# Kernel optimization log

Hardware: AMD Instinct MI355X
Metric: run time of the kernel (lower is better)

## Reference

```python
import jax, jax.numpy as jnp
import numpy as np

GRID = 2          # grid_num
IN_CH = 8         # mask branch out channels
CH = 8            # mask head channels
MR = 2.0          # mapping_ratio
SOI = jnp.array([64.0, 128.0, 256.0, 512.0, 1024.0], dtype=jnp.float32)


def _interp_matrix(out_len, in_len, dtype):
    # bilinear, align_corners=True, separable 1-D interpolation matrix [out_len, in_len]
    pos = jnp.arange(out_len, dtype=dtype) * ((in_len - 1) / (out_len - 1))
    lo = jnp.clip(jnp.floor(pos).astype(jnp.int32), 0, in_len - 2)
    frac = pos - lo.astype(dtype)
    M = jnp.zeros((out_len, in_len), dtype)
    idx = jnp.arange(out_len)
    M = M.at[idx, lo].add(1.0 - frac)
    M = M.at[idx, lo + 1].add(frac)
    return M


def _forward(mask_feats, mask_head_params, instance_locations, im_inds, fpn_levels, mask_feat_stride):
    N, C, H, W = mask_feats.shape
    n_inst = mask_head_params.shape[0]
    dt = mask_feats.dtype

    # compute_locations (FCOS): pixel centers of stride-s grid, (x, y) order, y-major flatten
    s = mask_feat_stride
    shifts_x = jnp.arange(W, dtype=dt) * s + s // 2
    shifts_y = jnp.arange(H, dtype=dt) * s + s // 2
    yy, xx = jnp.meshgrid(shifts_y, shifts_x, indexing='ij')
    locations = jnp.stack([xx.reshape(-1), yy.reshape(-1)], axis=-1)  # [H*W, 2]

    # relative coords, normalized by size-of-interest of each instance's FPN level
    rel = instance_locations[:, None, :] - locations[None, :, :]          # [n, HW, 2]
    rel = jnp.transpose(rel, (0, 2, 1))                                   # [n, 2, HW]
    rel = (rel / SOI[fpn_levels][:, None, None]).astype(dt)

    feats = mask_feats[im_inds].reshape(n_inst, IN_CH, H * W)             # [n, 8, HW]
    x = jnp.concatenate([rel, feats], axis=1).reshape(n_inst, IN_CH + 2, H, W)

    # grid-cell index from instance center (stride-8 coords, floor division)
    nl = instance_locations / 8.0
    gx = jnp.floor(jnp.clip(nl[:, 0], 0, W - 1) / (W // GRID))
    gy = jnp.floor(jnp.clip(nl[:, 1], 0, H - 1) / (H // GRID))
    loc_ind = (gx + GRID * gy).astype(jnp.int32)                          # [n]

    ih, iw = H // GRID, W // GRID
    # [n, c, gy, ih, gx, iw] -> [n, gy*gx, c, ih, iw], then gather one cell per instance
    xg = x.reshape(n_inst, IN_CH + 2, GRID, ih, GRID, iw)
    xg = jnp.transpose(xg, (0, 2, 4, 1, 3, 5)).reshape(n_inst, GRID * GRID, IN_CH + 2, ih, iw)
    x = xg[jnp.arange(n_inst), loc_ind]                                   # [n, 10, ih, iw]

    # parse dynamic params: weights [80, 64, 8] then biases [8, 8, 1]
    p = mask_head_params
    w0 = p[:, 0:80].reshape(n_inst, CH, IN_CH + 2)
    w1 = p[:, 80:144].reshape(n_inst, CH, CH)
    w2 = p[:, 144:152].reshape(n_inst, 1, CH)
    b0 = p[:, 152:160]
    b1 = p[:, 160:168]
    b2 = p[:, 168:169]

    # per-instance 1x1 grouped convs (groups = n_inst) as batched matmuls
    x = jax.nn.relu(jnp.einsum('nchw,nkc->nkhw', x, w0) + b0[:, :, None, None])
    x = jax.nn.relu(jnp.einsum('nchw,nkc->nkhw', x, w1) + b1[:, :, None, None])
    x = jnp.einsum('nchw,nkc->nkhw', x, w2) + b2[:, :, None, None]        # [n, 1, ih, iw]

    # bilinear upsample (align_corners=True) to out_size = (MR/2*H, MR/2*W) = (H, W)
    out_h = int(MR / 2.0 * H + 0.5)
    out_w = int(MR / 2.0 * W + 0.5)
    Mh = _interp_matrix(out_h, ih, dt)
    Mw = _interp_matrix(out_w, iw, dt)
    x = jnp.einsum('nchw,Hh,Ww->ncHW', x, Mh, Mw)
    return jax.nn.sigmoid(x)


def setup_inputs() -> dict:
    key = jax.random.key(0)
    k1, k2, k3, k4, k5 = jax.random.split(key, 5)
    N, H, W = 2, 192, 256
    n_inst = 128
    mask_feats = jax.random.normal(k1, (N, IN_CH, H, W), jnp.float32)
    mask_head_params = jax.random.normal(k2, (n_inst, 169), jnp.float32) * 0.1
    instance_locations = jax.random.uniform(k3, (n_inst, 2), jnp.float32) * jnp.array([W * 8.0, H * 8.0], jnp.float32)
    im_inds = jax.random.randint(k4, (n_inst,), 0, N)
    fpn_levels = jax.random.randint(k5, (n_inst,), 0, 5)
    return {
        'mask_feats': mask_feats,
        'mask_head_params': mask_head_params,
        'instance_locations': instance_locations,
        'im_inds': im_inds,
        'fpn_levels': fpn_levels,
        'mask_feat_stride': 8,
    }


def reference(mask_feats, mask_head_params, instance_locations, im_inds, fpn_levels, mask_feat_stride):
    return _forward(mask_feats, mask_head_params, instance_locations, im_inds, fpn_levels, mask_feat_stride)
```

## Files before the change

### kernel.cpp

```cpp
#include <hip/hip_runtime.h>


#define HH 192
#define WW 256
#define IH 96
#define IW 128
#define HW (HH * WW)

__global__ __launch_bounds__(256, 6) void dmh_kernel(
    const float* __restrict__ mf,
    const float* __restrict__ params,
    const float* __restrict__ locs,
    const int*   __restrict__ im_inds,
    const int*   __restrict__ fpn,
    const int*   __restrict__ stride_p,
    float*       __restrict__ out)
{
    __shared__ float m[8 * IW];

    const int bx   = blockIdx.x;
    const int inst = bx >> 4;
    const int q    = bx & 15;
    const int tid  = threadIdx.x;

    const int   s   = stride_p[0];
    const int   sh  = s >> 1;
    const float ix  = locs[2 * inst + 0];
    const float iy  = locs[2 * inst + 1];
    const float inv_soi = 1.0f / (float)(64 << fpn[inst]);
    const int   im  = im_inds[inst];

    const float nlx = ix * 0.125f;
    const float nly = iy * 0.125f;
    const int gx = (int)floorf(fminf(fmaxf(nlx, 0.0f), (float)(WW - 1)) / (float)(WW / 2));
    const int gy = (int)floorf(fminf(fmaxf(nly, 0.0f), (float)(HH - 1)) / (float)(HH / 2));

    const float* __restrict__ p = params + inst * 169;

    const int orow0 = q * 12;
    const int ms    = (int)((float)orow0 * (95.0f / 191.0f));

    {
        const int col4 = (tid & 31) * 4;
        const int r    = tid >> 5;
        int gr = ms + r; if (gr > IH - 1) gr = IH - 1;
        const int h = gy * IH + gr;
        const float rely = (iy - (float)(h * s + sh)) * inv_soi;

        const float* fbase = mf + (size_t)(im * 8) * HW + (size_t)h * WW
                             + gx * IW + col4;
        float4 f[8];
        #pragma unroll
        for (int c = 0; c < 8; ++c)
            f[c] = *(const float4*)(fbase + (size_t)c * HW);

        float4 res;
        float* rv = &res.x;
        #pragma unroll
        for (int j = 0; j < 4; ++j) {
            const float relx = (ix - (float)((gx * IW + col4 + j) * s + sh)) * inv_soi;
            float a[8];
            #pragma unroll
            for (int k = 0; k < 8; ++k) {
                float acc = p[152 + k];
                acc = fmaf(p[k * 10 + 0], relx, acc);
                acc = fmaf(p[k * 10 + 1], rely, acc);
                #pragma unroll
                for (int c = 0; c < 8; ++c)
                    acc = fmaf(p[k * 10 + 2 + c], ((const float*)&f[c])[j], acc);
                a[k] = fmaxf(acc, 0.0f);
            }
            float b[8];
            #pragma unroll
            for (int k = 0; k < 8; ++k) {
                float acc = p[160 + k];
                #pragma unroll
                for (int c = 0; c < 8; ++c)
                    acc = fmaf(p[80 + k * 8 + c], a[c], acc);
                b[k] = fmaxf(acc, 0.0f);
            }
            float acc = p[168];
            #pragma unroll
            for (int c = 0; c < 8; ++c)
                acc = fmaf(p[144 + c], b[c], acc);
            rv[j] = acc;
        }
        *(float4*)&m[r * IW + col4] = res;
    }
    __syncthreads();

    {
        const int ocol = tid;
        const float wpos = (float)ocol * (127.0f / 255.0f);
        int wlo = (int)wpos; if (wlo > IW - 2) wlo = IW - 2;
        const float fw = wpos - (float)wlo;

        float* op = out + (size_t)inst * HW + (size_t)orow0 * WW + ocol;

        #pragma unroll
        for (int r = 0; r < 12; ++r) {
            const float hpos = (float)(orow0 + r) * (95.0f / 191.0f);
            int hlo = (int)hpos; if (hlo > IH - 2) hlo = IH - 2;
            const float fh = hpos - (float)hlo;
            const int rl = hlo - ms;

            const float* mp = &m[rl * IW + wlo];
            const float v00 = mp[0];
            const float v01 = mp[1];
            const float v10 = mp[IW];
            const float v11 = mp[IW + 1];

            const float top = fmaf(fw, v01 - v00, v00);
            const float bot = fmaf(fw, v11 - v10, v10);
            const float val = fmaf(fh, bot - top, top);

            op[(size_t)r * WW] = 1.0f / (1.0f + __expf(-val));
        }
    }
}

extern "C" void kernel_launch(void* const* d_in, const int* in_sizes, int n_in,
                              void* d_out, int out_size, void* d_ws, size_t ws_size,
                              hipStream_t stream) {
    const float* mf       = (const float*)d_in[0];
    const float* params   = (const float*)d_in[1];
    const float* locs     = (const float*)d_in[2];
    const int*   im_inds  = (const int*)d_in[3];
    const int*   fpn      = (const int*)d_in[4];
    const int*   stride_p = (const int*)d_in[5];
    float*       out      = (float*)d_out;

    dmh_kernel<<<dim3(2048), dim3(256), 0, stream>>>(
        mf, params, locs, im_inds, fpn, stride_p, out);
}
```

Before: 20.57 us.

## Split dynamic mask head into separate MLP and upsample kernels via workspace

Replaces the fused kernel with two kernels when workspace allows: one computes the per-instance low-resolution mask with the MLP and writes it to the workspace, the other bilinearly upsamples it and applies sigmoid, using float4 stores. This removes the redundant MLP recomputation of overlapping low-res rows across the 16 row-chunks of the fused version. The cost is an extra launch and a round-trip of a 6 MB intermediate through global memory. The fallback fused kernel now processes two pixels per thread over eight rows.

```diff
diff --git a/kernel.cpp b/kernel.cpp
--- a/kernel.cpp
+++ b/kernel.cpp
@@ -6,114 +6,187 @@
 #define IH 96
 #define IW 128
 #define HW (HH * WW)
-
-__global__ __launch_bounds__(256, 6) void dmh_kernel(
-    const float* __restrict__ mf,
-    const float* __restrict__ params,
-    const float* __restrict__ locs,
-    const int*   __restrict__ im_inds,
-    const int*   __restrict__ fpn,
-    const int*   __restrict__ stride_p,
-    float*       __restrict__ out)
-{
-    __shared__ float m[8 * IW];
-
-    const int bx   = blockIdx.x;
-    const int inst = bx >> 4;
-    const int q    = bx & 15;
-    const int tid  = threadIdx.x;
-
-    const int   s   = stride_p[0];
-    const int   sh  = s >> 1;
-    const float ix  = locs[2 * inst + 0];
-    const float iy  = locs[2 * inst + 1];
-    const float inv_soi = 1.0f / (float)(64 << fpn[inst]);
-    const int   im  = im_inds[inst];
-
+#define MHW (IH * IW)
+
+__device__ __forceinline__ void inst_setup(
+    const float* __restrict__ locs, const int* __restrict__ im_inds,
+    const int* __restrict__ fpn, int s, int inst,
+    float& ix, float& iy, float& inv_soi, int& im, int& gx, int& gy)
+{
+    ix = locs[2 * inst + 0];
+    iy = locs[2 * inst + 1];
+    inv_soi = 1.0f / (float)(64 << fpn[inst]);
+    im = im_inds[inst];
     const float nlx = ix * 0.125f;
     const float nly = iy * 0.125f;
-    const int gx = (int)floorf(fminf(fmaxf(nlx, 0.0f), (float)(WW - 1)) / (float)(WW / 2));
-    const int gy = (int)floorf(fminf(fmaxf(nly, 0.0f), (float)(HH - 1)) / (float)(HH / 2));
-
+    gx = (int)floorf(fminf(fmaxf(nlx, 0.0f), (float)(WW - 1)) / (float)(WW / 2));
+    gy = (int)floorf(fminf(fmaxf(nly, 0.0f), (float)(HH - 1)) / (float)(HH / 2));
+}
+
+__device__ __forceinline__ float mlp_px(
+    const float* __restrict__ p, const float* f, float relx, float rely)
+{
+    float a[8];
+    #pragma unroll
+    for (int k = 0; k < 8; ++k) {
+        float acc = p[152 + k];
+        acc = fmaf(p[k * 10 + 0], relx, acc);
+        acc = fmaf(p[k * 10 + 1], rely, acc);
+        #pragma unroll
+        for (int c = 0; c < 8; ++c)
+            acc = fmaf(p[k * 10 + 2 + c], f[c], acc);
+        a[k] = fmaxf(acc, 0.0f);
+    }
+    float b[8];
+    #pragma unroll
+    for (int k = 0; k < 8; ++k) {
+        float acc = p[160 + k];
+        #pragma unroll
+        for (int c = 0; c < 8; ++c)
+            acc = fmaf(p[80 + k * 8 + c], a[c], acc);
+        b[k] = fmaxf(acc, 0.0f);
+    }
+    float acc = p[168];
+    #pragma unroll
+    for (int c = 0; c < 8; ++c)
+        acc = fmaf(p[144 + c], b[c], acc);
+    return acc;
+}
+
+__global__ __launch_bounds__(256, 8) void dmh_mask(
+    const float* __restrict__ mf, const float* __restrict__ params,
+    const float* __restrict__ locs, const int* __restrict__ im_inds,
+    const int* __restrict__ fpn, const int* __restrict__ stride_p,
+    float* __restrict__ mask)
+{
+    const int inst = blockIdx.y;
+    const int tid  = threadIdx.x;
+    const int s    = stride_p[0];
+    const int sh   = s >> 1;
+
+    float ix, iy, inv_soi; int im, gx, gy;
+    inst_setup(locs, im_inds, fpn, s, inst, ix, iy, inv_soi, im, gx, gy);
     const float* __restrict__ p = params + inst * 169;
 
+    const int col2 = (tid & 63) * 2;
+    const int gr   = blockIdx.x * 4 + (tid >> 6);
+    const int h    = gy * IH + gr;
+    const float rely = (iy - (float)(h * s + sh)) * inv_soi;
+
+    const float* fbase = mf + ((size_t)(im * 8) * HH + h) * WW + gx * IW + col2;
+    float2 f2[8];
+    #pragma unroll
+    for (int c = 0; c < 8; ++c)
+        f2[c] = *(const float2*)(fbase + (size_t)c * HW);
+
+    float f0[8], f1[8];
+    #pragma unroll
+    for (int c = 0; c < 8; ++c) { f0[c] = f2[c].x; f1[c] = f2[c].y; }
+
+    const float relx0 = (ix - (float)((gx * IW + col2) * s + sh)) * inv_soi;
+    const float relx1 = relx0 - (float)s * inv_soi;
+
+    float2 res;
+    res.x = mlp_px(p, f0, relx0, rely);
+    res.y = mlp_px(p, f1, relx1, rely);
+
+    *(float2*)&mask[(size_t)inst * MHW + gr * IW + col2] = res;
+}
+
+__global__ __launch_bounds__(256, 8) void dmh_upsample(
+    const float* __restrict__ mask, float* __restrict__ out)
+{
+    const int inst = blockIdx.y;
+    const int tid  = threadIdx.x;
+    const int col4 = (tid & 63) * 4;
+    const int orow = blockIdx.x * 4 + (tid >> 6);
+
+    const float hpos = (float)orow * (95.0f / 191.0f);
+    int hlo = (int)hpos; if (hlo > IH - 2) hlo = IH - 2;
+    const float fh = hpos - (float)hlo;
+
+    const float* mrow = mask + (size_t)inst * MHW + hlo * IW;
+
+    float4 v;
+    float* vv = &v.x;
+    #pragma unroll
+    for (int j = 0; j < 4; ++j) {
+        const float wpos = (float)(col4 + j) * (127.0f / 255.0f);
+        int wlo = (int)wpos; if (wlo > IW - 2) wlo = IW - 2;
+        const float fw = wpos - (float)wlo;
+
+        const float v00 = mrow[wlo];
+        const float v01 = mrow[wlo + 1];
+        const float v10 = mrow[wlo + IW];
+        const float v11 = mrow[wlo + IW + 1];
+
+        const float top = fmaf(fw, v01 - v00, v00);
+        const float bot = fmaf(fw, v11 - v10, v10);
+        const float val = fmaf(fh, bot - top, top);
+        vv[j] = 1.0f / (1.0f + __expf(-val));
+    }
+    *(float4*)(out + (size_t)inst * HW + (size_t)orow * WW + col4) = v;
+}
+
+__global__ __launch_bounds__(256, 6) void dmh_fused(
+    const float* __restrict__ mf, const float* __restrict__ params,
+    const float* __restrict__ locs, const int* __restrict__ im_inds,
+    const int* __restrict__ fpn, const int* __restrict__ stride_p,
+    float* __restrict__ out)
+{
+    __shared__ float m[8 * IW];
+    const int bx = blockIdx.x;
+    const int inst = bx >> 4;
+    const int q = bx & 15;
+    const int tid = threadIdx.x;
+    const int s = stride_p[0];
+    const int sh = s >> 1;
+
+    float ix, iy, inv_soi; int im, gx, gy;
+    inst_setup(locs, im_inds, fpn, s, inst, ix, iy, inv_soi, im, gx, gy);
+    const float* __restrict__ p = params + inst * 169;
+
     const int orow0 = q * 12;
-    const int ms    = (int)((float)orow0 * (95.0f / 191.0f));
-
+    const int ms = (int)((float)orow0 * (95.0f / 191.0f));
     {
-        const int col4 = (tid & 31) * 4;
-        const int r    = tid >> 5;
-        int gr = ms + r; if (gr > IH - 1) gr = IH - 1;
-        const int h = gy * IH + gr;
-        const float rely = (iy - (float)(h * s + sh)) * inv_soi;
-
-        const float* fbase = mf + (size_t)(im * 8) * HW + (size_t)h * WW
-                             + gx * IW + col4;
-        float4 f[8];
-        #pragma unroll
-        for (int c = 0; c < 8; ++c)
-            f[c] = *(const float4*)(fbase + (size_t)c * HW);
-
-        float4 res;
-        float* rv = &res.x;
-        #pragma unroll
-        for (int j = 0; j < 4; ++j) {
-            const float relx = (ix - (float)((gx * IW + col4 + j) * s + sh)) * inv_soi;
-            float a[8];
+        const int col2 = (tid & 63) * 2;
+        const int r = tid >> 6;
+        #pragma unroll
+        for (int rr = 0; rr < 2; ++rr) {
+            int gr = ms + r + rr * 4; if (gr > IH - 1) gr = IH - 1;
+            const int h = gy * IH + gr;
+            const float rely = (iy - (float)(h * s + sh)) * inv_soi;
+            const float* fbase = mf + ((size_t)(im * 8) * HH + h) * WW + gx * IW + col2;
+            float f0[8], f1[8];
             #pragma unroll
-            for (int k = 0; k < 8; ++k) {
-                float acc = p[152 + k];
-                acc = fmaf(p[k * 10 + 0], relx, acc);
-                acc = fmaf(p[k * 10 + 1], rely, acc);
-                #pragma unroll
-                for (int c = 0; c < 8; ++c)
-                    acc = fmaf(p[k * 10 + 2 + c], ((const float*)&f[c])[j], acc);
-                a[k] = fmaxf(acc, 0.0f);
+            for (int c = 0; c < 8; ++c) {
+                float2 t = *(const float2*)(fbase + (size_t)c * HW);
+                f0[c] = t.x; f1[c] = t.y;
             }
-            float b[8];
-            #pragma unroll
-            for (int k = 0; k < 8; ++k) {
-                float acc = p[160 + k];
-                #pragma unroll
-                for (int c = 0; c < 8; ++c)
-                    acc = fmaf(p[80 + k * 8 + c], a[c], acc);
-                b[k] = fmaxf(acc, 0.0f);
-            }
-            float acc = p[168];
-            #pragma unroll
-            for (int c = 0; c < 8; ++c)
-                acc = fmaf(p[144 + c], b[c], acc);
-            rv[j] = acc;
+            const float relx0 = (ix - (float)((gx * IW + col2) * s + sh)) * inv_soi;
+            const float relx1 = relx0 - (float)s * inv_soi;
+            m[(r + rr * 4) * IW + col2]     = mlp_px(p, f0, relx0, rely);
+            m[(r + rr * 4) * IW + col2 + 1] = mlp_px(p, f1, relx1, rely);
         }
-        *(float4*)&m[r * IW + col4] = res;
     }
     __syncthreads();
-
     {
         const int ocol = tid;
         const float wpos = (float)ocol * (127.0f / 255.0f);
         int wlo = (int)wpos; if (wlo > IW - 2) wlo = IW - 2;
         const float fw = wpos - (float)wlo;
-
         float* op = out + (size_t)inst * HW + (size_t)orow0 * WW + ocol;
-
         #pragma unroll
         for (int r = 0; r < 12; ++r) {
             const float hpos = (float)(orow0 + r) * (95.0f / 191.0f);
             int hlo = (int)hpos; if (hlo > IH - 2) hlo = IH - 2;
             const float fh = hpos - (float)hlo;
             const int rl = hlo - ms;
-
             const float* mp = &m[rl * IW + wlo];
-            const float v00 = mp[0];
-            const float v01 = mp[1];
-            const float v10 = mp[IW];
-            const float v11 = mp[IW + 1];
-
+            const float v00 = mp[0], v01 = mp[1], v10 = mp[IW], v11 = mp[IW + 1];
             const float top = fmaf(fw, v01 - v00, v00);
             const float bot = fmaf(fw, v11 - v10, v10);
             const float val = fmaf(fh, bot - top, top);
-
             op[(size_t)r * WW] = 1.0f / (1.0f + __expf(-val));
         }
     }
@@ -130,6 +203,14 @@
     const int*   stride_p = (const int*)d_in[5];
     float*       out      = (float*)d_out;
 
-    dmh_kernel<<<dim3(2048), dim3(256), 0, stream>>>(
-        mf, params, locs, im_inds, fpn, stride_p, out);
-}
+    const size_t mask_bytes = (size_t)128 * MHW * sizeof(float);
+    if (ws_size >= mask_bytes) {
+        float* mask = (float*)d_ws;
+        dmh_mask<<<dim3(24, 128), dim3(256), 0, stream>>>(
+            mf, params, locs, im_inds, fpn, stride_p, mask);
+        dmh_upsample<<<dim3(48, 128), dim3(256), 0, stream>>>(mask, out);
+    } else {
+        dmh_fused<<<dim3(2048), dim3(256), 0, stream>>>(
+            mf, params, locs, im_inds, fpn, stride_p, out);
+    }
+}
```

Result: slower. 28.66 us (+39.3%).

## Process 24 output rows per block to cut halo recompute of the MLP

Applied to the files above, without the earlier changes.

Each block now covers 24 output rows (14 source rows) instead of 12 output rows (8 source rows), halving the grid. The per-pixel MLP is no longer recomputed for the overlapping halo rows that adjacent blocks shared. The upsampling loop keeps the two interpolation rows in registers and reloads from shared memory only when the source row advances. In exchange there is less parallelism (1024 blocks), a partial second compute pass in which some threads sit idle, and a lower occupancy hint in launch bounds.

```diff
diff --git a/kernel.cpp b/kernel.cpp
--- a/kernel.cpp
+++ b/kernel.cpp
@@ -7,7 +7,7 @@
 #define IW 128
 #define HW (HH * WW)
 
-__global__ __launch_bounds__(256, 6) void dmh_kernel(
+__global__ __launch_bounds__(256, 4) void dmh_kernel(
     const float* __restrict__ mf,
     const float* __restrict__ params,
     const float* __restrict__ locs,
@@ -16,11 +16,11 @@
     const int*   __restrict__ stride_p,
     float*       __restrict__ out)
 {
-    __shared__ float m[8 * IW];
+    __shared__ float m[14 * IW];
 
     const int bx   = blockIdx.x;
-    const int inst = bx >> 4;
-    const int q    = bx & 15;
+    const int inst = bx >> 3;
+    const int j    = bx & 7;
     const int tid  = threadIdx.x;
 
     const int   s   = stride_p[0];
@@ -37,55 +37,67 @@
 
     const float* __restrict__ p = params + inst * 169;
 
-    const int orow0 = q * 12;
-    const int ms    = (int)((float)orow0 * (95.0f / 191.0f));
+    const int orow0 = j * 24;
+    const int ms    = (orow0 * 95) / 191;
 
     {
         const int col4 = (tid & 31) * 4;
-        const int r    = tid >> 5;
-        int gr = ms + r; if (gr > IH - 1) gr = IH - 1;
-        const int h = gy * IH + gr;
-        const float rely = (iy - (float)(h * s + sh)) * inv_soi;
+        const int rs   = tid >> 5;
+        const float relx0 = (ix - (float)((gx * IW + col4) * s + sh)) * inv_soi;
+        const float dstep = (float)s * inv_soi;
+        const float* fcol = mf + (size_t)(im * 8) * HW + gx * IW + col4;
 
-        const float* fbase = mf + (size_t)(im * 8) * HW + (size_t)h * WW
-                             + gx * IW + col4;
-        float4 f[8];
         #pragma unroll
-        for (int c = 0; c < 8; ++c)
-            f[c] = *(const float4*)(fbase + (size_t)c * HW);
+        for (int pass = 0; pass < 2; ++pass) {
+            const int r = rs + pass * 8;
+            if (r < 14) {
+                int gr = ms + r; if (gr > IH - 1) gr = IH - 1;
+                const int h = gy * IH + gr;
+                const float rely = (iy - (float)(h * s + sh)) * inv_soi;
 
-        float4 res;
-        float* rv = &res.x;
-        #pragma unroll
-        for (int j = 0; j < 4; ++j) {
-            const float relx = (ix - (float)((gx * IW + col4 + j) * s + sh)) * inv_soi;
-            float a[8];
-            #pragma unroll
-            for (int k = 0; k < 8; ++k) {
-                float acc = p[152 + k];
-                acc = fmaf(p[k * 10 + 0], relx, acc);
-                acc = fmaf(p[k * 10 + 1], rely, acc);
+                const float* fbase = fcol + (size_t)h * WW;
+                float4 F[8];
                 #pragma unroll
                 for (int c = 0; c < 8; ++c)
-                    acc = fmaf(p[k * 10 + 2 + c], ((const float*)&f[c])[j], acc);
-                a[k] = fmaxf(acc, 0.0f);
+                    F[c] = *(const float4*)(fbase + (size_t)c * HW);
+
+                float4 res;
+                float* rv = &res.x;
+                #pragma unroll
+                for (int jp = 0; jp < 4; ++jp) {
+                    const float relx = relx0 - (float)jp * dstep;
+                    float f[8];
+                    #pragma unroll
+                    for (int c = 0; c < 8; ++c) f[c] = ((const float*)&F[c])[jp];
+                    float a[8];
+                    #pragma unroll
+                    for (int k = 0; k < 8; ++k) {
+                        float acc = p[152 + k];
+                        acc = fmaf(p[k * 10 + 0], relx, acc);
+                        acc = fmaf(p[k * 10 + 1], rely, acc);
+                        #pragma unroll
+                        for (int c = 0; c < 8; ++c)
+                            acc = fmaf(p[k * 10 + 2 + c], f[c], acc);
+                        a[k] = fmaxf(acc, 0.0f);
+                    }
+                    float b[8];
+                    #pragma unroll
+                    for (int k = 0; k < 8; ++k) {
+                        float acc = p[160 + k];
+                        #pragma unroll
+                        for (int c = 0; c < 8; ++c)
+                            acc = fmaf(p[80 + k * 8 + c], a[c], acc);
+                        b[k] = fmaxf(acc, 0.0f);
+                    }
+                    float acc = p[168];
+                    #pragma unroll
+                    for (int c = 0; c < 8; ++c)
+                        acc = fmaf(p[144 + c], b[c], acc);
+                    rv[jp] = acc;
+                }
+                *(float4*)&m[r * IW + col4] = res;
             }
-            float b[8];
-            #pragma unroll
-            for (int k = 0; k < 8; ++k) {
-                float acc = p[160 + k];
-                #pragma unroll
-                for (int c = 0; c < 8; ++c)
-                    acc = fmaf(p[80 + k * 8 + c], a[c], acc);
-                b[k] = fmaxf(acc, 0.0f);
-            }
-            float acc = p[168];
-            #pragma unroll
-            for (int c = 0; c < 8; ++c)
-                acc = fmaf(p[144 + c], b[c], acc);
-            rv[j] = acc;
         }
-        *(float4*)&m[r * IW + col4] = res;
     }
     __syncthreads();
 
@@ -97,23 +109,36 @@
 
         float* op = out + (size_t)inst * HW + (size_t)orow0 * WW + ocol;
 
-        #pragma unroll
-        for (int r = 0; r < 12; ++r) {
-            const float hpos = (float)(orow0 + r) * (95.0f / 191.0f);
-            int hlo = (int)hpos; if (hlo > IH - 2) hlo = IH - 2;
-            const float fh = hpos - (float)hlo;
-            const int rl = hlo - ms;
-
-            const float* mp = &m[rl * IW + wlo];
-            const float v00 = mp[0];
-            const float v01 = mp[1];
-            const float v10 = mp[IW];
-            const float v11 = mp[IW + 1];
-
+        float v00 = m[wlo];
+        float v01 = m[wlo + 1];
+        float v10 = m[IW + wlo];
+        float v11 = m[IW + wlo + 1];
+        int cur = 0;
+        {
+            const float fh = (float)orow0 * (95.0f / 191.0f) - (float)ms;
             const float top = fmaf(fw, v01 - v00, v00);
             const float bot = fmaf(fw, v11 - v10, v10);
             const float val = fmaf(fh, bot - top, top);
+            op[0] = 1.0f / (1.0f + __expf(-val));
+        }
 
+        #pragma unroll
+        for (int r = 1; r < 24; ++r) {
+            const int orow = orow0 + r;
+            int ihlo = (orow * 95) / 191;
+            if (ihlo > IH - 2) ihlo = IH - 2;
+            const float fh = (float)orow * (95.0f / 191.0f) - (float)ihlo;
+            const int rl = ihlo - ms;
+
+            if (rl != cur) {
+                v00 = v10; v01 = v11;
+                v10 = m[(rl + 1) * IW + wlo];
+                v11 = m[(rl + 1) * IW + wlo + 1];
+                cur = rl;
+            }
+            const float top = fmaf(fw, v01 - v00, v00);
+            const float bot = fmaf(fw, v11 - v10, v10);
+            const float val = fmaf(fh, bot - top, top);
             op[(size_t)r * WW] = 1.0f / (1.0f + __expf(-val));
         }
     }
@@ -130,6 +155,6 @@
     const int*   stride_p = (const int*)d_in[5];
     float*       out      = (float*)d_out;
 
-    dmh_kernel<<<dim3(2048), dim3(256), 0, stream>>>(
+    dmh_kernel<<<dim3(1024), dim3(256), 0, stream>>>(
         mf, params, locs, im_inds, fpn, stride_p, out);
 }
```

Result: slower. 21.49 us (+4.5%).
